# Optimization experiments

Measured on AMD Instinct MI355X. Metric: run time of the kernel, lower is better.

## Reference

```python
import jax, jax.numpy as jnp
import numpy as np

N_NODES = 100000
N_FEAT = 256
HIDDEN = 32
N_EDGES = 3200000


def setup_inputs() -> dict:
    key = jax.random.key(0)
    ks = jax.random.split(key, 12)
    in_dim = N_FEAT + HIDDEN  # DConv gates take cat([X, H]) of width F+32
    scale = 1.0 / np.sqrt(in_dim)
    def gate_w(k):
        # DConv weight has shape (2, K=1, in_dim, out_dim)
        return jax.random.uniform(k, (2, 1, in_dim, HIDDEN), jnp.float32, -scale, scale)
    return {
        "x": jax.random.normal(ks[0], (N_NODES, N_FEAT), jnp.float32),
        "edge_index": jax.random.randint(ks[1], (2, N_EDGES), 0, N_NODES, jnp.int64),
        "edge_weight": jax.random.uniform(ks[2], (N_EDGES,), jnp.float32),
        "Wz": gate_w(ks[3]), "bz": jnp.zeros((HIDDEN,), jnp.float32),
        "Wr": gate_w(ks[4]), "br": jnp.zeros((HIDDEN,), jnp.float32),
        "Wh": gate_w(ks[5]), "bh": jnp.zeros((HIDDEN,), jnp.float32),
        "Wlin": jax.random.normal(ks[6], (HIDDEN, 1), jnp.float32) / np.sqrt(HIDDEN),
        "blin": jnp.zeros((1,), jnp.float32),
    }


def _dconv_k1(inp, W, b):
    # K=1 diffusion conv: only the 0-hop term fires in torch_geometric_temporal's
    # DConv (the propagate branch requires weight.size(1) > 1), so
    # H = inp @ W[0,0] + inp @ W[1,0] + b  (edge_index/edge_weight unused).
    return inp @ (W[0, 0] + W[1, 0]) + b


def reference(x, edge_index, edge_weight, Wz, bz, Wr, br, Wh, bh, Wlin, blin):
    N = x.shape[0]
    H0 = jnp.zeros((N, HIDDEN), x.dtype)  # _set_hidden_state with H=None
    cat = jnp.concatenate([x, H0], axis=1)            # [N, F+32]
    Z = jax.nn.sigmoid(_dconv_k1(cat, Wz, bz))        # update gate
    R = jax.nn.sigmoid(_dconv_k1(cat, Wr, br))        # reset gate
    cat_h = jnp.concatenate([x, H0 * R], axis=1)
    H_tilde = jnp.tanh(_dconv_k1(cat_h, Wh, bh))      # candidate state
    H = Z * H0 + (1.0 - Z) * H_tilde                  # GRU hidden update
    h = jax.nn.relu(H)
    return h @ Wlin + blin                            # [N, 1]
```

## Files before the change

kernel.cpp:

```cpp
#include <hip/hip_runtime.h>
#include <hip/hip_bf16.h>

#define NN 100000
#define NF 256


typedef short bf16x8 __attribute__((ext_vector_type(8)));
typedef float f32x4 __attribute__((ext_vector_type(4)));

__device__ __forceinline__ unsigned short f2bf_rne(float f) {
  unsigned u = __float_as_uint(f);
  return (unsigned short)((u + 0x7fffu + ((u >> 16) & 1u)) >> 16);
}
__device__ __forceinline__ float bf2f(unsigned short h) {
  return __uint_as_float(((unsigned)h) << 16);
}

__global__ __launch_bounds__(256) void prep_kernel(
    const float* __restrict__ Wz, const float* __restrict__ Wh,
    unsigned short* __restrict__ ws) {
  const int i = blockIdx.x * 256 + threadIdx.x;
  const int j = i & 7;
  const int lane = (i >> 3) & 63;
  const int tile = i >> 9;
  const int kt = tile >> 2;
  const int ct = tile & 3;
  const int col = ct * 16 + (lane & 15);
  const int k = kt * 32 + ((lane >> 4) & 3) * 8 + j;
  const int jj = col & 31;
  const float* W = (col < 32) ? Wz : Wh;
  const float v = W[k * 32 + jj] + W[9216 + k * 32 + jj];
  const unsigned short hi = f2bf_rne(v);
  const unsigned short lo = f2bf_rne(v - bf2f(hi));
  ws[i] = hi;
  ws[16384 + i] = lo;
}

__global__ __launch_bounds__(256) void main_kernel(
    const float* __restrict__ x,
    const unsigned short* __restrict__ ws,
    const float* __restrict__ Wlin, const float* __restrict__ blin,
    float* __restrict__ out) {
  const int tid = threadIdx.x;
  const int lane = tid & 63;
  const int c = lane & 15;
  const int q = lane >> 4;
  const int nb = blockIdx.x * 64 + (tid >> 6) * 16;

  int row = nb + c;
  if (row >= NN) row = NN - 1;
  const float* __restrict__ xr = x + (size_t)row * NF;

  f32x4 acc[4] = {{0.f, 0.f, 0.f, 0.f}, {0.f, 0.f, 0.f, 0.f},
                  {0.f, 0.f, 0.f, 0.f}, {0.f, 0.f, 0.f, 0.f}};

  const bf16x8* __restrict__ wsH = (const bf16x8*)ws;
  const bf16x8* __restrict__ wsL = (const bf16x8*)(ws + 16384);

#pragma unroll
  for (int kt = 0; kt < 8; ++kt) {
    const float4* __restrict__ xp = (const float4*)(xr + kt * 32 + q * 8);
    const float4 f0 = xp[0];
    const float4 f1 = xp[1];
    const float fv[8] = {f0.x, f0.y, f0.z, f0.w, f1.x, f1.y, f1.z, f1.w};
    bf16x8 xh, xl;
#pragma unroll
    for (int j = 0; j < 8; ++j) {
      const unsigned short h = f2bf_rne(fv[j]);
      xh[j] = (short)h;
      xl[j] = (short)f2bf_rne(fv[j] - bf2f(h));
    }
#pragma unroll
    for (int ct = 0; ct < 4; ++ct) {
      const bf16x8 bh = wsH[(kt * 4 + ct) * 64 + lane];
      const bf16x8 bl = wsL[(kt * 4 + ct) * 64 + lane];
      acc[ct] = __builtin_amdgcn_mfma_f32_16x16x32_bf16(xh, bh, acc[ct], 0, 0, 0);
      acc[ct] = __builtin_amdgcn_mfma_f32_16x16x32_bf16(xl, bh, acc[ct], 0, 0, 0);
      acc[ct] = __builtin_amdgcn_mfma_f32_16x16x32_bf16(xh, bl, acc[ct], 0, 0, 0);
    }
  }

  float part[4] = {0.f, 0.f, 0.f, 0.f};
#pragma unroll
  for (int p = 0; p < 2; ++p) {
    const float wl = Wlin[c + 16 * p];
#pragma unroll
    for (int r = 0; r < 4; ++r) {
      const float z = 1.f / (1.f + expf(-acc[p][r]));
      const float th = tanhf(acc[2 + p][r]);
      const float h = fmaxf((1.f - z) * th, 0.f);
      part[r] = fmaf(h, wl, part[r]);
    }
  }
#pragma unroll
  for (int d = 1; d < 16; d <<= 1) {
#pragma unroll
    for (int r = 0; r < 4; ++r) part[r] += __shfl_xor(part[r], d);
  }
  if (c == 0) {
    const float b0 = blin[0];
#pragma unroll
    for (int r = 0; r < 4; ++r) {
      const int node = nb + q * 4 + r;
      if (node < NN) out[node] = part[r] + b0;
    }
  }
}

extern "C" void kernel_launch(void* const* d_in, const int* in_sizes, int n_in,
                              void* d_out, int out_size, void* d_ws, size_t ws_size,
                              hipStream_t stream) {
  const float* x    = (const float*)d_in[0];
  const float* Wz   = (const float*)d_in[3];
  const float* Wh   = (const float*)d_in[7];
  const float* Wlin = (const float*)d_in[9];
  const float* blin = (const float*)d_in[10];
  unsigned short* ws = (unsigned short*)d_ws;
  float* out = (float*)d_out;

  prep_kernel<<<64, 256, 0, stream>>>(Wz, Wh, ws);
  main_kernel<<<(NN + 63) / 64, 256, 0, stream>>>(x, ws, Wlin, blin, out);
}
```

Baseline: 200.2 us.

## Stage split weights in LDS, process two row tiles per wave, cheaper bf16 split

The block now copies the 64KB of hi/lo bf16 weights into shared memory once, and each wave handles 32 rows instead of 16, so every weight fragment read serves two MFMA row tiles. The fp32-to-bf16 hi/lo split now uses truncation with byte permutes instead of round-to-nearest arithmetic. Together these cut weight loads and conversion ALU work per row. The cost is 64KB of LDS per block, which limits occupancy and so the latency hiding for the streaming x reads. Truncation also shifts the error of the split slightly.

```diff
diff --git a/kernel.cpp b/kernel.cpp
--- a/kernel.cpp
+++ b/kernel.cpp
@@ -6,6 +6,7 @@
 
 
 typedef short bf16x8 __attribute__((ext_vector_type(8)));
+typedef int i32x4 __attribute__((ext_vector_type(4)));
 typedef float f32x4 __attribute__((ext_vector_type(4)));
 
 __device__ __forceinline__ unsigned short f2bf_rne(float f) {
@@ -36,73 +37,111 @@
   ws[16384 + i] = lo;
 }
 
+__device__ __forceinline__ void split8(const float4 f0, const float4 f1,
+                                       bf16x8& xh, bf16x8& xl) {
+  unsigned u[8] = {__float_as_uint(f0.x), __float_as_uint(f0.y),
+                   __float_as_uint(f0.z), __float_as_uint(f0.w),
+                   __float_as_uint(f1.x), __float_as_uint(f1.y),
+                   __float_as_uint(f1.z), __float_as_uint(f1.w)};
+  i32x4 ph, pl;
+#pragma unroll
+  for (int j = 0; j < 4; ++j)
+    ph[j] = (int)__builtin_amdgcn_perm(u[2 * j + 1], u[2 * j], 0x07060302u);
+  unsigned r[8];
+#pragma unroll
+  for (int j = 0; j < 8; ++j)
+    r[j] = __float_as_uint(__uint_as_float(u[j]) -
+                           __uint_as_float(u[j] & 0xffff0000u));
+#pragma unroll
+  for (int j = 0; j < 4; ++j)
+    pl[j] = (int)__builtin_amdgcn_perm(r[2 * j + 1], r[2 * j], 0x07060302u);
+  xh = __builtin_bit_cast(bf16x8, ph);
+  xl = __builtin_bit_cast(bf16x8, pl);
+}
+
 __global__ __launch_bounds__(256) void main_kernel(
     const float* __restrict__ x,
     const unsigned short* __restrict__ ws,
     const float* __restrict__ Wlin, const float* __restrict__ blin,
     float* __restrict__ out) {
+  __shared__ alignas(16) unsigned short sB[32768];
+
   const int tid = threadIdx.x;
+  {
+    const uint4* __restrict__ g = (const uint4*)ws;
+    uint4* __restrict__ s = (uint4*)sB;
+#pragma unroll
+    for (int i = 0; i < 16; ++i) s[tid + i * 256] = g[tid + i * 256];
+  }
+  __syncthreads();
+
   const int lane = tid & 63;
   const int c = lane & 15;
   const int q = lane >> 4;
-  const int nb = blockIdx.x * 64 + (tid >> 6) * 16;
+  const int nbw = blockIdx.x * 128 + (tid >> 6) * 32;
 
-  int row = nb + c;
-  if (row >= NN) row = NN - 1;
-  const float* __restrict__ xr = x + (size_t)row * NF;
+  int row0 = nbw + c;       if (row0 >= NN) row0 = NN - 1;
+  int row1 = nbw + 16 + c;  if (row1 >= NN) row1 = NN - 1;
+  const float* __restrict__ xr0 = x + (size_t)row0 * NF;
+  const float* __restrict__ xr1 = x + (size_t)row1 * NF;
 
-  f32x4 acc[4] = {{0.f, 0.f, 0.f, 0.f}, {0.f, 0.f, 0.f, 0.f},
-                  {0.f, 0.f, 0.f, 0.f}, {0.f, 0.f, 0.f, 0.f}};
+  const bf16x8* __restrict__ BH = (const bf16x8*)sB;
+  const bf16x8* __restrict__ BL = (const bf16x8*)(sB + 16384);
 
-  const bf16x8* __restrict__ wsH = (const bf16x8*)ws;
-  const bf16x8* __restrict__ wsL = (const bf16x8*)(ws + 16384);
+  f32x4 acc[2][4] = {{{0.f, 0.f, 0.f, 0.f}, {0.f, 0.f, 0.f, 0.f},
+                      {0.f, 0.f, 0.f, 0.f}, {0.f, 0.f, 0.f, 0.f}},
+                     {{0.f, 0.f, 0.f, 0.f}, {0.f, 0.f, 0.f, 0.f},
+                      {0.f, 0.f, 0.f, 0.f}, {0.f, 0.f, 0.f, 0.f}}};
 
 #pragma unroll
   for (int kt = 0; kt < 8; ++kt) {
-    const float4* __restrict__ xp = (const float4*)(xr + kt * 32 + q * 8);
-    const float4 f0 = xp[0];
-    const float4 f1 = xp[1];
-    const float fv[8] = {f0.x, f0.y, f0.z, f0.w, f1.x, f1.y, f1.z, f1.w};
-    bf16x8 xh, xl;
-#pragma unroll
-    for (int j = 0; j < 8; ++j) {
-      const unsigned short h = f2bf_rne(fv[j]);
-      xh[j] = (short)h;
-      xl[j] = (short)f2bf_rne(fv[j] - bf2f(h));
-    }
+    const float4* __restrict__ xp0 = (const float4*)(xr0 + kt * 32 + q * 8);
+    const float4* __restrict__ xp1 = (const float4*)(xr1 + kt * 32 + q * 8);
+    bf16x8 xh[2], xl[2];
+    split8(xp0[0], xp0[1], xh[0], xl[0]);
+    split8(xp1[0], xp1[1], xh[1], xl[1]);
 #pragma unroll
     for (int ct = 0; ct < 4; ++ct) {
-      const bf16x8 bh = wsH[(kt * 4 + ct) * 64 + lane];
-      const bf16x8 bl = wsL[(kt * 4 + ct) * 64 + lane];
-      acc[ct] = __builtin_amdgcn_mfma_f32_16x16x32_bf16(xh, bh, acc[ct], 0, 0, 0);
-      acc[ct] = __builtin_amdgcn_mfma_f32_16x16x32_bf16(xl, bh, acc[ct], 0, 0, 0);
-      acc[ct] = __builtin_amdgcn_mfma_f32_16x16x32_bf16(xh, bl, acc[ct], 0, 0, 0);
+      const bf16x8 bh = BH[(kt * 4 + ct) * 64 + lane];
+      const bf16x8 bl = BL[(kt * 4 + ct) * 64 + lane];
+#pragma unroll
+      for (int rt = 0; rt < 2; ++rt) {
+        acc[rt][ct] =
+            __builtin_amdgcn_mfma_f32_16x16x32_bf16(xh[rt], bh, acc[rt][ct], 0, 0, 0);
+        acc[rt][ct] =
+            __builtin_amdgcn_mfma_f32_16x16x32_bf16(xl[rt], bh, acc[rt][ct], 0, 0, 0);
+        acc[rt][ct] =
+            __builtin_amdgcn_mfma_f32_16x16x32_bf16(xh[rt], bl, acc[rt][ct], 0, 0, 0);
+      }
     }
   }
 
-  float part[4] = {0.f, 0.f, 0.f, 0.f};
+  const float b0 = blin[0];
 #pragma unroll
-  for (int p = 0; p < 2; ++p) {
-    const float wl = Wlin[c + 16 * p];
+  for (int rt = 0; rt < 2; ++rt) {
+    float part[4] = {0.f, 0.f, 0.f, 0.f};
 #pragma unroll
-    for (int r = 0; r < 4; ++r) {
-      const float z = 1.f / (1.f + expf(-acc[p][r]));
-      const float th = tanhf(acc[2 + p][r]);
-      const float h = fmaxf((1.f - z) * th, 0.f);
-      part[r] = fmaf(h, wl, part[r]);
+    for (int p = 0; p < 2; ++p) {
+      const float wl = Wlin[c + 16 * p];
+#pragma unroll
+      for (int r = 0; r < 4; ++r) {
+        const float z = 1.f / (1.f + expf(-acc[rt][p][r]));
+        const float th = tanhf(acc[rt][2 + p][r]);
+        const float h = fmaxf((1.f - z) * th, 0.f);
+        part[r] = fmaf(h, wl, part[r]);
+      }
     }
-  }
 #pragma unroll
-  for (int d = 1; d < 16; d <<= 1) {
+    for (int d = 1; d < 16; d <<= 1) {
 #pragma unroll
-    for (int r = 0; r < 4; ++r) part[r] += __shfl_xor(part[r], d);
-  }
-  if (c == 0) {
-    const float b0 = blin[0];
+      for (int r = 0; r < 4; ++r) part[r] += __shfl_xor(part[r], d);
+    }
+    if (c == 0) {
 #pragma unroll
-    for (int r = 0; r < 4; ++r) {
-      const int node = nb + q * 4 + r;
-      if (node < NN) out[node] = part[r] + b0;
+      for (int r = 0; r < 4; ++r) {
+        const int node = nbw + rt * 16 + q * 4 + r;
+        if (node < NN) out[node] = part[r] + b0;
+      }
     }
   }
 }
@@ -119,5 +158,5 @@
   float* out = (float*)d_out;
 
   prep_kernel<<<64, 256, 0, stream>>>(Wz, Wh, ws);
-  main_kernel<<<(NN + 63) / 64, 256, 0, stream>>>(x, ws, Wlin, blin, out);
+  main_kernel<<<(NN + 127) / 128, 256, 0, stream>>>(x, ws, Wlin, blin, out);
 }
```

New measurement: 198.6 us. Within noise of the previous version (-0.8%).
